# Optimization experiments

Hardware: AMD Instinct MI355X
Metric: run time of the kernel (lower is better)

The kernel has to match this reference:

```python
import jax, jax.numpy as jnp
import numpy as np


def setup_inputs() -> dict:
    key = jax.random.key(0)
    k1, k2, k3, k4 = jax.random.split(key, 4)
    B, C_in, C_out, E, K = 4, 128, 256, 30000, 5
    x = jax.random.normal(k1, (B, C_in, E, 1), dtype=jnp.float32)
    ne_idx = jax.random.randint(k2, (B, E, K - 1), 0, E, dtype=jnp.int32)
    conv_w = jax.random.normal(k3, (C_out, C_in, 1, K), dtype=jnp.float32) * 0.05
    conv_b = jax.random.normal(k4, (C_out,), dtype=jnp.float32) * 0.05
    return {"x": x, "ne_idx": ne_idx, "conv_w": conv_w, "conv_b": conv_b}


def reference(x, ne_idx, conv_w, conv_b):
    # x: [B, C, E, 1] edge features; ne_idx: [B, E, 4] neighbor edge ids.
    B, C, E, _ = x.shape
    xs = x[..., 0]                                        # [B, C, E]

    # pad_graph_mat: prepend self index column -> [B, E, 5]
    self_idx = jnp.broadcast_to(
        jnp.arange(E, dtype=ne_idx.dtype)[None, :, None], (B, E, 1))
    idx = jnp.concatenate([self_idx, ne_idx], axis=2) + 1  # +1 for zero pad slot

    # zero-pad feature dim so index 0 maps to zeros (matches torch padding col)
    x_pad = jnp.pad(xs, ((0, 0), (0, 0), (1, 0)))          # [B, C, E+1]

    # gather: f[b, c, e, k] = x_pad[b, c, idx[b, e, k]]
    f = jax.vmap(lambda xp, i: xp[:, i])(x_pad, idx)       # [B, C, E, 5]

    e0, e1, e2, e3, e4 = (f[..., j] for j in range(5))
    p = e1 + e3
    q = e2 + e4
    p1 = jnp.abs(e1 - e3)
    q1 = jnp.abs(e2 - e4)
    G = jnp.stack([e0, p, q, p1, q1], axis=-1)             # [B, C, E, 5]

    # Conv2d with kernel (1, 5): contraction over in-channels and the 5 taps
    out = jnp.einsum('bcek,ocuk->boe', G, conv_w) + conv_b[None, :, None]
    return out[..., None]                                  # [B, C_out, E, 1]
```

## Files before the change

### kernel.cpp

```cpp
#include <hip/hip_runtime.h>
#include <hip/hip_bf16.h>
#include <stdint.h>

#define E_N   30000
#define C_IN  128
#define C_OUT 256
#define B_N   4
#define KTAP  5
#define BN    64

typedef short bf16x8 __attribute__((ext_vector_type(8)));
typedef float f32x4  __attribute__((ext_vector_type(4)));

static __device__ __forceinline__ unsigned short f2bf(float f) {
    union { float f; uint32_t u; } v; v.f = f;
    uint32_t r = (v.u + 0x7FFFu + ((v.u >> 16) & 1u)) >> 16;
    return (unsigned short)r;
}
static __device__ __forceinline__ float bf2f(uint32_t h) {
    union { uint32_t u; float f; } v; v.u = h << 16;
    return v.f;
}

static __device__ __forceinline__ void comb8(const uint4& u, const uint4& v,
                                             uint4& s, uint4& d) {
    const uint32_t* a = (const uint32_t*)&u;
    const uint32_t* b = (const uint32_t*)&v;
    uint32_t* so = (uint32_t*)&s;
    uint32_t* dr = (uint32_t*)&d;
#pragma unroll
    for (int i = 0; i < 4; ++i) {
        float x0 = bf2f(a[i] & 0xFFFFu), x1 = bf2f(a[i] >> 16);
        float y0 = bf2f(b[i] & 0xFFFFu), y1 = bf2f(b[i] >> 16);
        so[i] = (uint32_t)f2bf(x0 + y0) | ((uint32_t)f2bf(x1 + y1) << 16);
        dr[i] = (uint32_t)f2bf(fabsf(x0 - y0)) | ((uint32_t)f2bf(fabsf(x1 - y1)) << 16);
    }
}

__global__ void pack_w_kernel(const float* __restrict__ w,
                              unsigned short* __restrict__ wp) {
    int tid = blockIdx.x * blockDim.x + threadIdx.x;
    if (tid >= 20 * 16 * 64) return;
    int s    = tid >> 10;
    int mt   = (tid >> 6) & 15;
    int lane = tid & 63;
    int m    = mt * 16 + (lane & 15);
    int kb   = s * 32 + ((lane >> 4) & 3) * 8;
    uint32_t pv[4];
    for (int jj = 0; jj < 4; ++jj) {
        unsigned short lo, hi;
        {
            int kk = kb + 2 * jj;
            int t = kk >> 7, c = kk & 127;
            lo = f2bf(w[(m * C_IN + c) * KTAP + t]);
        }
        {
            int kk = kb + 2 * jj + 1;
            int t = kk >> 7, c = kk & 127;
            hi = f2bf(w[(m * C_IN + c) * KTAP + t]);
        }
        pv[jj] = (uint32_t)lo | ((uint32_t)hi << 16);
    }
    uint4 val; val.x = pv[0]; val.y = pv[1]; val.z = pv[2]; val.w = pv[3];
    *(uint4*)(wp + (size_t)tid * 8) = val;
}

__global__ void transpose_kernel(const float* __restrict__ x,
                                 unsigned short* __restrict__ xT) {
    __shared__ float ld[C_IN][64 + 1];
    int b  = blockIdx.y;
    int e0 = blockIdx.x * 64;
    int t  = threadIdx.x;
    bool full = (e0 + 64 <= E_N);
    for (int pass = 0; pass < 8; ++pass) {
        int c  = pass * 16 + (t >> 4);
        int eo = (t & 15) * 4;
        if (full) {
            const float4 v = *(const float4*)(x + ((size_t)(b * C_IN + c) * E_N + e0 + eo));
            ld[c][eo] = v.x; ld[c][eo + 1] = v.y; ld[c][eo + 2] = v.z; ld[c][eo + 3] = v.w;
        } else {
            for (int i = 0; i < 4; ++i) {
                int e = e0 + eo + i;
                ld[c][eo + i] = (e < E_N) ? x[(size_t)(b * C_IN + c) * E_N + e] : 0.f;
            }
        }
    }
    __syncthreads();
    for (int pass = 0; pass < 4; ++pass) {
        int el = pass * 16 + (t >> 4);
        int c0 = (t & 15) * 8;
        int e  = e0 + el;
        if (e < E_N) {
            uint32_t pk[4];
            for (int i = 0; i < 4; ++i) {
                unsigned short lo = f2bf(ld[c0 + 2 * i][el]);
                unsigned short hi = f2bf(ld[c0 + 2 * i + 1][el]);
                pk[i] = (uint32_t)lo | ((uint32_t)hi << 16);
            }
            uint4 v; v.x = pk[0]; v.y = pk[1]; v.z = pk[2]; v.w = pk[3];
            *(uint4*)(xT + (size_t)(b * E_N + e) * C_IN + c0) = v;
        }
    }
}

__launch_bounds__(512, 4)
__global__ void mesh_gemm(const unsigned short* __restrict__ wp,
                          const unsigned short* __restrict__ xT,
                          const int* __restrict__ ne,
                          const float* __restrict__ bias,
                          float* __restrict__ out) {
    __shared__ uint4 gbuf[KTAP][BN][16];

    const int e0   = blockIdx.x * BN;
    const int tid  = threadIdx.x;
    const int lane = tid & 63;
    const int wave = tid >> 6;
    const int b0   = blockIdx.y * 2;
    const int b1   = b0 + 1;

    const int col = tid >> 3;
    const int ci  = tid & 7;
    int eg = e0 + col; if (eg >= E_N) eg = E_N - 1;

    const int4 nb0 = *(const int4*)(ne + ((size_t)b0 * E_N + eg) * 4);
    const int4 nb1 = *(const int4*)(ne + ((size_t)b1 * E_N + eg) * 4);

    const int sw = col & 15;
    const int cl = ci ^ sw;
    const int ch = (ci + 8) ^ sw;

    const uint4* wp16 = (const uint4*)wp;
    const int nl   = lane & 15;
    const int kq   = lane >> 4;
    const int quad = kq;

    float bvl[2][4];
#pragma unroll
    for (int mt = 0; mt < 2; ++mt)
#pragma unroll
        for (int r = 0; r < 4; ++r)
            bvl[mt][r] = bias[(wave * 2 + mt) * 16 + quad * 4 + r];

    auto gather10 = [&](int b, const int4& nb, uint4* g) {
        const unsigned short* xb = xT + (size_t)b * E_N * C_IN;
        const uint4* r0 = (const uint4*)(xb + (size_t)eg   * C_IN) + ci;
        const uint4* r1 = (const uint4*)(xb + (size_t)nb.x * C_IN) + ci;
        const uint4* r2 = (const uint4*)(xb + (size_t)nb.y * C_IN) + ci;
        const uint4* r3 = (const uint4*)(xb + (size_t)nb.z * C_IN) + ci;
        const uint4* r4 = (const uint4*)(xb + (size_t)nb.w * C_IN) + ci;
        g[0] = r0[0]; g[1] = r1[0]; g[2] = r2[0]; g[3] = r3[0]; g[4] = r4[0];
        g[5] = r0[8]; g[6] = r1[8]; g[7] = r2[8]; g[8] = r3[8]; g[9] = r4[8];
    };
    auto combineStore = [&](uint4* g) {
        uint4 s, d;
        gbuf[0][col][cl] = g[0];
        comb8(g[1], g[3], s, d); gbuf[1][col][cl] = s; gbuf[3][col][cl] = d;
        comb8(g[2], g[4], s, d); gbuf[2][col][cl] = s; gbuf[4][col][cl] = d;
        gbuf[0][col][ch] = g[5];
        comb8(g[6], g[8], s, d); gbuf[1][col][ch] = s; gbuf[3][col][ch] = d;
        comb8(g[7], g[9], s, d); gbuf[2][col][ch] = s; gbuf[4][col][ch] = d;
    };
    auto mfmaStore = [&](int b) {
        f32x4 acc[2][4];
#pragma unroll
        for (int mt = 0; mt < 2; ++mt)
#pragma unroll
            for (int nt = 0; nt < 4; ++nt)
                acc[mt][nt] = (f32x4){0.f, 0.f, 0.f, 0.f};
#pragma unroll 4
        for (int s = 0; s < 20; ++s) {
            const int tap = s >> 2, cbi = s & 3;
            uint4 w0 = wp16[(s * 16 + wave * 2 + 0) * 64 + lane];
            uint4 w1 = wp16[(s * 16 + wave * 2 + 1) * 64 + lane];
            bf16x8 af0 = *(bf16x8*)&w0;
            bf16x8 af1 = *(bf16x8*)&w1;
#pragma unroll
            for (int nt = 0; nt < 4; ++nt) {
                uint4 bv = gbuf[tap][nt * 16 + nl][((cbi << 2) + kq) ^ nl];
                bf16x8 bf = *(bf16x8*)&bv;
                acc[0][nt] = __builtin_amdgcn_mfma_f32_16x16x32_bf16(af0, bf, acc[0][nt], 0, 0, 0);
                acc[1][nt] = __builtin_amdgcn_mfma_f32_16x16x32_bf16(af1, bf, acc[1][nt], 0, 0, 0);
            }
        }
#pragma unroll
        for (int mt = 0; mt < 2; ++mt) {
            const int ob = (wave * 2 + mt) * 16 + quad * 4;
#pragma unroll
            for (int r = 0; r < 4; ++r) {
                const int o = ob + r;
                const float bv = bvl[mt][r];
#pragma unroll
                for (int nt = 0; nt < 4; ++nt) {
                    const int e = e0 + nt * 16 + nl;
                    if (e < E_N)
                        out[((size_t)(b * C_OUT + o)) * E_N + e] = acc[mt][nt][r] + bv;
                }
            }
        }
    };

    uint4 ga[10];
    gather10(b0, nb0, ga);
    combineStore(ga);
    __syncthreads();

    uint4 gb[10];
    gather10(b1, nb1, gb);
    mfmaStore(b0);

    __syncthreads();
    combineStore(gb);
    __syncthreads();
    mfmaStore(b1);
}

__global__ void fallback_kernel(const float* __restrict__ x,
                                const int* __restrict__ ne,
                                const float* __restrict__ w,
                                const float* __restrict__ bias,
                                float* __restrict__ out) {
    size_t id = (size_t)blockIdx.x * blockDim.x + threadIdx.x;
    if (id >= (size_t)B_N * C_OUT * E_N) return;
    int e = (int)(id % E_N);
    int o = (int)((id / E_N) % C_OUT);
    int b = (int)(id / ((size_t)E_N * C_OUT));
    const int4 nb = *(const int4*)(ne + ((size_t)b * E_N + e) * 4);
    float acc = bias[o];
    for (int c = 0; c < C_IN; ++c) {
        const float* xb = x + (size_t)(b * C_IN + c) * E_N;
        float s0 = xb[e];
        float x1 = xb[nb.x], x2 = xb[nb.y], x3 = xb[nb.z], x4 = xb[nb.w];
        const float* wo = w + (size_t)(o * C_IN + c) * KTAP;
        acc += wo[0] * s0
             + wo[1] * (x1 + x3)
             + wo[2] * (x2 + x4)
             + wo[3] * fabsf(x1 - x3)
             + wo[4] * fabsf(x2 - x4);
    }
    out[id] = acc;
}

extern "C" void kernel_launch(void* const* d_in, const int* in_sizes, int n_in,
                              void* d_out, int out_size, void* d_ws, size_t ws_size,
                              hipStream_t stream) {
    const float* x      = (const float*)d_in[0];
    const int*   ne_idx = (const int*)d_in[1];
    const float* conv_w = (const float*)d_in[2];
    const float* conv_b = (const float*)d_in[3];
    float* out = (float*)d_out;

    const size_t xT_off = 512 * 1024;
    const size_t need   = xT_off + (size_t)B_N * E_N * C_IN * 2;

    if (ws_size < need) {
        size_t total = (size_t)B_N * C_OUT * E_N;
        int blocks = (int)((total + 255) / 256);
        fallback_kernel<<<blocks, 256, 0, stream>>>(x, ne_idx, conv_w, conv_b, out);
        return;
    }

    unsigned short* wp = (unsigned short*)d_ws;
    unsigned short* xT = (unsigned short*)((char*)d_ws + xT_off);

    pack_w_kernel<<<80, 256, 0, stream>>>(conv_w, wp);
    dim3 tg((E_N + 63) / 64, B_N);
    transpose_kernel<<<tg, 256, 0, stream>>>(x, xT);
    dim3 gg((E_N + BN - 1) / BN, B_N / 2);
    mesh_gemm<<<gg, 512, 0, stream>>>(wp, xT, ne_idx, conv_b, out);
}
```

Measured before the change: 231.8 us.

## Make mesh_gemm persistent with register-cached weights and software-pipelined gathers

The GEMM kernel now runs as a persistent grid of 512 blocks. Each block loops over (edge-tile, batch) work items in strides of GRIDX and overlaps the gather of the next tile, plus prefetch of its neighbor indices, with the MFMA loop on the current tile. 16 of the 20 weight fragments per wave are loaded once into registers instead of being re-read from global memory every tile, and launch bounds drop to 2 blocks per CU to make room for them. The cost is much higher register pressure and lower occupancy. The fixed 512-block grid also loses the previous per-block reuse of edge indices across two batches.

```diff
diff --git a/kernel.cpp b/kernel.cpp
--- a/kernel.cpp
+++ b/kernel.cpp
@@ -8,6 +8,7 @@
 #define B_N   4
 #define KTAP  5
 #define BN    64
+#define GRIDX 512
 
 typedef short bf16x8 __attribute__((ext_vector_type(8)));
 typedef float f32x4  __attribute__((ext_vector_type(4)));
@@ -103,7 +104,7 @@
     }
 }
 
-__launch_bounds__(512, 4)
+__launch_bounds__(512, 2)
 __global__ void mesh_gemm(const unsigned short* __restrict__ wp,
                           const unsigned short* __restrict__ xT,
                           const int* __restrict__ ne,
@@ -111,38 +112,46 @@
                           float* __restrict__ out) {
     __shared__ uint4 gbuf[KTAP][BN][16];
 
-    const int e0   = blockIdx.x * BN;
     const int tid  = threadIdx.x;
     const int lane = tid & 63;
     const int wave = tid >> 6;
-    const int b0   = blockIdx.y * 2;
-    const int b1   = b0 + 1;
+    const int bq   = blockIdx.x & 3;
+    const int NQ   = ((E_N + BN - 1) / BN) * B_N;
 
     const int col = tid >> 3;
     const int ci  = tid & 7;
-    int eg = e0 + col; if (eg >= E_N) eg = E_N - 1;
-
-    const int4 nb0 = *(const int4*)(ne + ((size_t)b0 * E_N + eg) * 4);
-    const int4 nb1 = *(const int4*)(ne + ((size_t)b1 * E_N + eg) * 4);
-
-    const int sw = col & 15;
-    const int cl = ci ^ sw;
-    const int ch = (ci + 8) ^ sw;
+    const int sw  = col & 15;
+    const int cl  = ci ^ sw;
+    const int ch  = (ci + 8) ^ sw;
+
+    const unsigned short* xb   = xT  + (size_t)bq * E_N * C_IN;
+    const int*            neb  = ne  + (size_t)bq * E_N * 4;
+    float*                outb = out + (size_t)bq * C_OUT * E_N;
 
     const uint4* wp16 = (const uint4*)wp;
-    const int nl   = lane & 15;
-    const int kq   = lane >> 4;
-    const int quad = kq;
+    const int nl = lane & 15;
+    const int kq = lane >> 4;
+
+    uint4 wc0[16], wc1[16];
+#pragma unroll
+    for (int s = 0; s < 16; ++s) {
+        wc0[s] = wp16[(s * 16 + wave * 2 + 0) * 64 + lane];
+        wc1[s] = wp16[(s * 16 + wave * 2 + 1) * 64 + lane];
+    }
 
     float bvl[2][4];
 #pragma unroll
     for (int mt = 0; mt < 2; ++mt)
 #pragma unroll
         for (int r = 0; r < 4; ++r)
-            bvl[mt][r] = bias[(wave * 2 + mt) * 16 + quad * 4 + r];
-
-    auto gather10 = [&](int b, const int4& nb, uint4* g) {
-        const unsigned short* xb = xT + (size_t)b * E_N * C_IN;
+            bvl[mt][r] = bias[(wave * 2 + mt) * 16 + kq * 4 + r];
+
+    auto egOf = [&](int q) {
+        int e = (q >> 2) * BN + col;
+        return (e < E_N) ? e : (E_N - 1);
+    };
+
+    auto gather10 = [&](int eg, const int4& nb, uint4* g) {
         const uint4* r0 = (const uint4*)(xb + (size_t)eg   * C_IN) + ci;
         const uint4* r1 = (const uint4*)(xb + (size_t)nb.x * C_IN) + ci;
         const uint4* r2 = (const uint4*)(xb + (size_t)nb.y * C_IN) + ci;
@@ -160,20 +169,18 @@
         comb8(g[6], g[8], s, d); gbuf[1][col][ch] = s; gbuf[3][col][ch] = d;
         comb8(g[7], g[9], s, d); gbuf[2][col][ch] = s; gbuf[4][col][ch] = d;
     };
-    auto mfmaStore = [&](int b) {
+    auto mfmaStore = [&](int et) {
         f32x4 acc[2][4];
 #pragma unroll
         for (int mt = 0; mt < 2; ++mt)
 #pragma unroll
             for (int nt = 0; nt < 4; ++nt)
                 acc[mt][nt] = (f32x4){0.f, 0.f, 0.f, 0.f};
-#pragma unroll 4
-        for (int s = 0; s < 20; ++s) {
+#pragma unroll
+        for (int s = 0; s < 16; ++s) {
             const int tap = s >> 2, cbi = s & 3;
-            uint4 w0 = wp16[(s * 16 + wave * 2 + 0) * 64 + lane];
-            uint4 w1 = wp16[(s * 16 + wave * 2 + 1) * 64 + lane];
-            bf16x8 af0 = *(bf16x8*)&w0;
-            bf16x8 af1 = *(bf16x8*)&w1;
+            bf16x8 af0 = *(bf16x8*)&wc0[s];
+            bf16x8 af1 = *(bf16x8*)&wc1[s];
 #pragma unroll
             for (int nt = 0; nt < 4; ++nt) {
                 uint4 bv = gbuf[tap][nt * 16 + nl][((cbi << 2) + kq) ^ nl];
@@ -183,8 +190,24 @@
             }
         }
 #pragma unroll
+        for (int s = 16; s < 20; ++s) {
+            const int cbi = s & 3;
+            uint4 w0 = wp16[(s * 16 + wave * 2 + 0) * 64 + lane];
+            uint4 w1 = wp16[(s * 16 + wave * 2 + 1) * 64 + lane];
+            bf16x8 af0 = *(bf16x8*)&w0;
+            bf16x8 af1 = *(bf16x8*)&w1;
+#pragma unroll
+            for (int nt = 0; nt < 4; ++nt) {
+                uint4 bv = gbuf[4][nt * 16 + nl][((cbi << 2) + kq) ^ nl];
+                bf16x8 bf = *(bf16x8*)&bv;
+                acc[0][nt] = __builtin_amdgcn_mfma_f32_16x16x32_bf16(af0, bf, acc[0][nt], 0, 0, 0);
+                acc[1][nt] = __builtin_amdgcn_mfma_f32_16x16x32_bf16(af1, bf, acc[1][nt], 0, 0, 0);
+            }
+        }
+        const int e0 = et * BN;
+#pragma unroll
         for (int mt = 0; mt < 2; ++mt) {
-            const int ob = (wave * 2 + mt) * 16 + quad * 4;
+            const int ob = (wave * 2 + mt) * 16 + kq * 4;
 #pragma unroll
             for (int r = 0; r < 4; ++r) {
                 const int o = ob + r;
@@ -193,25 +216,46 @@
                 for (int nt = 0; nt < 4; ++nt) {
                     const int e = e0 + nt * 16 + nl;
                     if (e < E_N)
-                        out[((size_t)(b * C_OUT + o)) * E_N + e] = acc[mt][nt][r] + bv;
+                        outb[(size_t)o * E_N + e] = acc[mt][nt][r] + bv;
                 }
             }
         }
     };
 
-    uint4 ga[10];
-    gather10(b0, nb0, ga);
-    combineStore(ga);
+    uint4 g[10];
+    int q = blockIdx.x;
+    {
+        int eg = egOf(q);
+        int4 nb = *(const int4*)(neb + (size_t)eg * 4);
+        gather10(eg, nb, g);
+    }
+    int qg = q + GRIDX;
+    int egN = 0; int4 nbN = {0, 0, 0, 0};
+    if (qg < NQ) { egN = egOf(qg); nbN = *(const int4*)(neb + (size_t)egN * 4); }
+
+    combineStore(g);
+    if (qg < NQ) {
+        gather10(egN, nbN, g);
+        int qp = qg + GRIDX;
+        if (qp < NQ) { egN = egOf(qp); nbN = *(const int4*)(neb + (size_t)egN * 4); }
+    }
     __syncthreads();
 
-    uint4 gb[10];
-    gather10(b1, nb1, gb);
-    mfmaStore(b0);
-
-    __syncthreads();
-    combineStore(gb);
-    __syncthreads();
-    mfmaStore(b1);
+    for (;;) {
+        mfmaStore(q >> 2);
+        __syncthreads();
+        const int qc = q + GRIDX;
+        if (qc >= NQ) break;
+        combineStore(g);
+        const int qg2 = qc + GRIDX;
+        if (qg2 < NQ) {
+            gather10(egN, nbN, g);
+            const int qp = qg2 + GRIDX;
+            if (qp < NQ) { egN = egOf(qp); nbN = *(const int4*)(neb + (size_t)egN * 4); }
+        }
+        __syncthreads();
+        q = qc;
+    }
 }
 
 __global__ void fallback_kernel(const float* __restrict__ x,
@@ -265,6 +309,5 @@
     pack_w_kernel<<<80, 256, 0, stream>>>(conv_w, wp);
     dim3 tg((E_N + 63) / 64, B_N);
     transpose_kernel<<<tg, 256, 0, stream>>>(x, xT);
-    dim3 gg((E_N + BN - 1) / BN, B_N / 2);
-    mesh_gemm<<<gg, 512, 0, stream>>>(wp, xT, ne_idx, conv_b, out);
-}
+    mesh_gemm<<<dim3(GRIDX), 512, 0, stream>>>(wp, xT, ne_idx, conv_b, out);
+}
```

Measured after the change: 310.6 us. 1.34x slower.

## Gather both batches into double LDS buffer and share weight loads across batches

Applied to the files above, without the earlier changes.

Both batch items' neighbor gathers are now issued up front into a doubled shared buffer, and a single MFMA loop computes both batches, so each weight fragment loaded from global memory is reused twice. This removes the serialized gather/compute/sync sequence and halves weight reloads. The cost is double the LDS footprint (about 80KB) and twice the accumulator registers, so occupancy is pinned to 2 waves per EU, and latency hiding that came from overlapping the second gather with the first compute is lost.

```diff
diff --git a/kernel.cpp b/kernel.cpp
--- a/kernel.cpp
+++ b/kernel.cpp
@@ -103,46 +103,47 @@
     }
 }
 
-__launch_bounds__(512, 4)
+__launch_bounds__(512)
+__attribute__((amdgpu_waves_per_eu(2, 2)))
 __global__ void mesh_gemm(const unsigned short* __restrict__ wp,
                           const unsigned short* __restrict__ xT,
                           const int* __restrict__ ne,
                           const float* __restrict__ bias,
                           float* __restrict__ out) {
-    __shared__ uint4 gbuf[KTAP][BN][16];
-
-    const int e0   = blockIdx.x * BN;
+    __shared__ uint4 gbuf[2][KTAP][BN][16];
+
     const int tid  = threadIdx.x;
     const int lane = tid & 63;
     const int wave = tid >> 6;
+    const int e0   = blockIdx.x * BN;
     const int b0   = blockIdx.y * 2;
     const int b1   = b0 + 1;
 
     const int col = tid >> 3;
     const int ci  = tid & 7;
+    const int sw  = col & 15;
+    const int cl  = ci ^ sw;
+    const int ch  = (ci + 8) ^ sw;
     int eg = e0 + col; if (eg >= E_N) eg = E_N - 1;
 
     const int4 nb0 = *(const int4*)(ne + ((size_t)b0 * E_N + eg) * 4);
     const int4 nb1 = *(const int4*)(ne + ((size_t)b1 * E_N + eg) * 4);
 
-    const int sw = col & 15;
-    const int cl = ci ^ sw;
-    const int ch = (ci + 8) ^ sw;
+    const unsigned short* xb0 = xT + (size_t)b0 * E_N * C_IN;
+    const unsigned short* xb1 = xT + (size_t)b1 * E_N * C_IN;
 
     const uint4* wp16 = (const uint4*)wp;
-    const int nl   = lane & 15;
-    const int kq   = lane >> 4;
-    const int quad = kq;
+    const int nl = lane & 15;
+    const int kq = lane >> 4;
 
     float bvl[2][4];
 #pragma unroll
     for (int mt = 0; mt < 2; ++mt)
 #pragma unroll
         for (int r = 0; r < 4; ++r)
-            bvl[mt][r] = bias[(wave * 2 + mt) * 16 + quad * 4 + r];
-
-    auto gather10 = [&](int b, const int4& nb, uint4* g) {
-        const unsigned short* xb = xT + (size_t)b * E_N * C_IN;
+            bvl[mt][r] = bias[(wave * 2 + mt) * 16 + kq * 4 + r];
+
+    auto gather10 = [&](const unsigned short* xb, const int4& nb, uint4* g) {
         const uint4* r0 = (const uint4*)(xb + (size_t)eg   * C_IN) + ci;
         const uint4* r1 = (const uint4*)(xb + (size_t)nb.x * C_IN) + ci;
         const uint4* r2 = (const uint4*)(xb + (size_t)nb.y * C_IN) + ci;
@@ -151,40 +152,61 @@
         g[0] = r0[0]; g[1] = r1[0]; g[2] = r2[0]; g[3] = r3[0]; g[4] = r4[0];
         g[5] = r0[8]; g[6] = r1[8]; g[7] = r2[8]; g[8] = r3[8]; g[9] = r4[8];
     };
-    auto combineStore = [&](uint4* g) {
+    auto combineStore = [&](const uint4* g, int bh) {
         uint4 s, d;
-        gbuf[0][col][cl] = g[0];
-        comb8(g[1], g[3], s, d); gbuf[1][col][cl] = s; gbuf[3][col][cl] = d;
-        comb8(g[2], g[4], s, d); gbuf[2][col][cl] = s; gbuf[4][col][cl] = d;
-        gbuf[0][col][ch] = g[5];
-        comb8(g[6], g[8], s, d); gbuf[1][col][ch] = s; gbuf[3][col][ch] = d;
-        comb8(g[7], g[9], s, d); gbuf[2][col][ch] = s; gbuf[4][col][ch] = d;
+        gbuf[bh][0][col][cl] = g[0];
+        comb8(g[1], g[3], s, d); gbuf[bh][1][col][cl] = s; gbuf[bh][3][col][cl] = d;
+        comb8(g[2], g[4], s, d); gbuf[bh][2][col][cl] = s; gbuf[bh][4][col][cl] = d;
+        gbuf[bh][0][col][ch] = g[5];
+        comb8(g[6], g[8], s, d); gbuf[bh][1][col][ch] = s; gbuf[bh][3][col][ch] = d;
+        comb8(g[7], g[9], s, d); gbuf[bh][2][col][ch] = s; gbuf[bh][4][col][ch] = d;
     };
-    auto mfmaStore = [&](int b) {
-        f32x4 acc[2][4];
+
+    {
+        uint4 g0[10], g1[10];
+        gather10(xb0, nb0, g0);
+        gather10(xb1, nb1, g1);
+        combineStore(g0, 0);
+        combineStore(g1, 1);
+    }
+    __syncthreads();
+
+    f32x4 acc[2][2][4];
+#pragma unroll
+    for (int bh = 0; bh < 2; ++bh)
 #pragma unroll
         for (int mt = 0; mt < 2; ++mt)
 #pragma unroll
             for (int nt = 0; nt < 4; ++nt)
-                acc[mt][nt] = (f32x4){0.f, 0.f, 0.f, 0.f};
+                acc[bh][mt][nt] = (f32x4){0.f, 0.f, 0.f, 0.f};
+
 #pragma unroll 4
-        for (int s = 0; s < 20; ++s) {
-            const int tap = s >> 2, cbi = s & 3;
-            uint4 w0 = wp16[(s * 16 + wave * 2 + 0) * 64 + lane];
-            uint4 w1 = wp16[(s * 16 + wave * 2 + 1) * 64 + lane];
-            bf16x8 af0 = *(bf16x8*)&w0;
-            bf16x8 af1 = *(bf16x8*)&w1;
-#pragma unroll
-            for (int nt = 0; nt < 4; ++nt) {
-                uint4 bv = gbuf[tap][nt * 16 + nl][((cbi << 2) + kq) ^ nl];
-                bf16x8 bf = *(bf16x8*)&bv;
-                acc[0][nt] = __builtin_amdgcn_mfma_f32_16x16x32_bf16(af0, bf, acc[0][nt], 0, 0, 0);
-                acc[1][nt] = __builtin_amdgcn_mfma_f32_16x16x32_bf16(af1, bf, acc[1][nt], 0, 0, 0);
-            }
-        }
+    for (int s = 0; s < 20; ++s) {
+        const int tap = s >> 2, cbi = s & 3;
+        uint4 w0 = wp16[(s * 16 + wave * 2 + 0) * 64 + lane];
+        uint4 w1 = wp16[(s * 16 + wave * 2 + 1) * 64 + lane];
+        bf16x8 af0 = *(bf16x8*)&w0;
+        bf16x8 af1 = *(bf16x8*)&w1;
+#pragma unroll
+        for (int nt = 0; nt < 4; ++nt) {
+            const int cidx = ((cbi << 2) + kq) ^ nl;
+            uint4 bv0 = gbuf[0][tap][nt * 16 + nl][cidx];
+            bf16x8 bf0 = *(bf16x8*)&bv0;
+            acc[0][0][nt] = __builtin_amdgcn_mfma_f32_16x16x32_bf16(af0, bf0, acc[0][0][nt], 0, 0, 0);
+            acc[0][1][nt] = __builtin_amdgcn_mfma_f32_16x16x32_bf16(af1, bf0, acc[0][1][nt], 0, 0, 0);
+            uint4 bv1 = gbuf[1][tap][nt * 16 + nl][cidx];
+            bf16x8 bf1 = *(bf16x8*)&bv1;
+            acc[1][0][nt] = __builtin_amdgcn_mfma_f32_16x16x32_bf16(af0, bf1, acc[1][0][nt], 0, 0, 0);
+            acc[1][1][nt] = __builtin_amdgcn_mfma_f32_16x16x32_bf16(af1, bf1, acc[1][1][nt], 0, 0, 0);
+        }
+    }
+
+#pragma unroll
+    for (int bh = 0; bh < 2; ++bh) {
+        float* outb = out + (size_t)(b0 + bh) * C_OUT * E_N;
 #pragma unroll
         for (int mt = 0; mt < 2; ++mt) {
-            const int ob = (wave * 2 + mt) * 16 + quad * 4;
+            const int ob = (wave * 2 + mt) * 16 + kq * 4;
 #pragma unroll
             for (int r = 0; r < 4; ++r) {
                 const int o = ob + r;
@@ -193,25 +215,11 @@
                 for (int nt = 0; nt < 4; ++nt) {
                     const int e = e0 + nt * 16 + nl;
                     if (e < E_N)
-                        out[((size_t)(b * C_OUT + o)) * E_N + e] = acc[mt][nt][r] + bv;
+                        outb[(size_t)o * E_N + e] = acc[bh][mt][nt][r] + bv;
                 }
             }
         }
-    };
-
-    uint4 ga[10];
-    gather10(b0, nb0, ga);
-    combineStore(ga);
-    __syncthreads();
-
-    uint4 gb[10];
-    gather10(b1, nb1, gb);
-    mfmaStore(b0);
-
-    __syncthreads();
-    combineStore(gb);
-    __syncthreads();
-    mfmaStore(b1);
+    }
 }
 
 __global__ void fallback_kernel(const float* __restrict__ x,
```

New measurement: 244.7 us. +5.6%, slower.

## Split gather into channel halves to halve LDS and registers, raise occupancy

Applied to the files above, without the earlier changes.

The shared gather buffer now holds only half of the input channels, and the single batch's work is processed as two K-halves accumulated into the same registers. Only five gathered vectors are live at a time instead of ten. This cuts LDS and VGPR use so more waves per EU fit (waves_per_eu 6), while the next half's global gather still overlaps the MFMA loop. MFMA sections get raised scheduling priority. The cost is twice as many block barriers and more frequent LDS round trips, and bias is now read at store time.

```diff
diff --git a/kernel.cpp b/kernel.cpp
--- a/kernel.cpp
+++ b/kernel.cpp
@@ -103,115 +103,130 @@
     }
 }
 
-__launch_bounds__(512, 4)
+__launch_bounds__(512)
+__attribute__((amdgpu_waves_per_eu(6)))
 __global__ void mesh_gemm(const unsigned short* __restrict__ wp,
                           const unsigned short* __restrict__ xT,
                           const int* __restrict__ ne,
                           const float* __restrict__ bias,
                           float* __restrict__ out) {
-    __shared__ uint4 gbuf[KTAP][BN][16];
-
-    const int e0   = blockIdx.x * BN;
+    __shared__ uint4 gbuf[KTAP][BN][8];
+
     const int tid  = threadIdx.x;
     const int lane = tid & 63;
     const int wave = tid >> 6;
+    const int e0   = blockIdx.x * BN;
     const int b0   = blockIdx.y * 2;
-    const int b1   = b0 + 1;
 
     const int col = tid >> 3;
     const int ci  = tid & 7;
+    const int cs  = ci ^ (col & 7);
     int eg = e0 + col; if (eg >= E_N) eg = E_N - 1;
 
-    const int4 nb0 = *(const int4*)(ne + ((size_t)b0 * E_N + eg) * 4);
-    const int4 nb1 = *(const int4*)(ne + ((size_t)b1 * E_N + eg) * 4);
-
-    const int sw = col & 15;
-    const int cl = ci ^ sw;
-    const int ch = (ci + 8) ^ sw;
+    const unsigned short* xb0 = xT + (size_t)b0 * E_N * C_IN;
+    const unsigned short* xb1 = xb0 + (size_t)E_N * C_IN;
 
     const uint4* wp16 = (const uint4*)wp;
-    const int nl   = lane & 15;
-    const int kq   = lane >> 4;
-    const int quad = kq;
-
-    float bvl[2][4];
-#pragma unroll
-    for (int mt = 0; mt < 2; ++mt)
-#pragma unroll
-        for (int r = 0; r < 4; ++r)
-            bvl[mt][r] = bias[(wave * 2 + mt) * 16 + quad * 4 + r];
-
-    auto gather10 = [&](int b, const int4& nb, uint4* g) {
-        const unsigned short* xb = xT + (size_t)b * E_N * C_IN;
-        const uint4* r0 = (const uint4*)(xb + (size_t)eg   * C_IN) + ci;
-        const uint4* r1 = (const uint4*)(xb + (size_t)nb.x * C_IN) + ci;
-        const uint4* r2 = (const uint4*)(xb + (size_t)nb.y * C_IN) + ci;
-        const uint4* r3 = (const uint4*)(xb + (size_t)nb.z * C_IN) + ci;
-        const uint4* r4 = (const uint4*)(xb + (size_t)nb.w * C_IN) + ci;
-        g[0] = r0[0]; g[1] = r1[0]; g[2] = r2[0]; g[3] = r3[0]; g[4] = r4[0];
-        g[5] = r0[8]; g[6] = r1[8]; g[7] = r2[8]; g[8] = r3[8]; g[9] = r4[8];
-    };
-    auto combineStore = [&](uint4* g) {
+    const int nl = lane & 15;
+    const int kq = lane >> 4;
+
+    auto gather5 = [&](const unsigned short* xb, const int4& nb, int h, uint4* g) {
+        const int off = ci + (h << 3);
+        g[0] = ((const uint4*)(xb + (size_t)eg   * C_IN))[off];
+        g[1] = ((const uint4*)(xb + (size_t)nb.x * C_IN))[off];
+        g[2] = ((const uint4*)(xb + (size_t)nb.y * C_IN))[off];
+        g[3] = ((const uint4*)(xb + (size_t)nb.z * C_IN))[off];
+        g[4] = ((const uint4*)(xb + (size_t)nb.w * C_IN))[off];
+    };
+    auto combineStore5 = [&](const uint4* g) {
         uint4 s, d;
-        gbuf[0][col][cl] = g[0];
-        comb8(g[1], g[3], s, d); gbuf[1][col][cl] = s; gbuf[3][col][cl] = d;
-        comb8(g[2], g[4], s, d); gbuf[2][col][cl] = s; gbuf[4][col][cl] = d;
-        gbuf[0][col][ch] = g[5];
-        comb8(g[6], g[8], s, d); gbuf[1][col][ch] = s; gbuf[3][col][ch] = d;
-        comb8(g[7], g[9], s, d); gbuf[2][col][ch] = s; gbuf[4][col][ch] = d;
-    };
-    auto mfmaStore = [&](int b) {
-        f32x4 acc[2][4];
-#pragma unroll
-        for (int mt = 0; mt < 2; ++mt)
-#pragma unroll
-            for (int nt = 0; nt < 4; ++nt)
-                acc[mt][nt] = (f32x4){0.f, 0.f, 0.f, 0.f};
+        gbuf[0][col][cs] = g[0];
+        comb8(g[1], g[3], s, d); gbuf[1][col][cs] = s; gbuf[3][col][cs] = d;
+        comb8(g[2], g[4], s, d); gbuf[2][col][cs] = s; gbuf[4][col][cs] = d;
+    };
+    auto mfmaHalf = [&](int h, f32x4 (&acc)[2][4]) {
+        __builtin_amdgcn_s_setprio(1);
 #pragma unroll 4
-        for (int s = 0; s < 20; ++s) {
-            const int tap = s >> 2, cbi = s & 3;
+        for (int p = 0; p < 10; ++p) {
+            const int tap = p >> 1, cbi2 = p & 1;
+            const int s = tap * 4 + (h << 1) + cbi2;
             uint4 w0 = wp16[(s * 16 + wave * 2 + 0) * 64 + lane];
             uint4 w1 = wp16[(s * 16 + wave * 2 + 1) * 64 + lane];
             bf16x8 af0 = *(bf16x8*)&w0;
             bf16x8 af1 = *(bf16x8*)&w1;
 #pragma unroll
             for (int nt = 0; nt < 4; ++nt) {
-                uint4 bv = gbuf[tap][nt * 16 + nl][((cbi << 2) + kq) ^ nl];
+                uint4 bv = gbuf[tap][nt * 16 + nl][((cbi2 << 2) + kq) ^ (nl & 7)];
                 bf16x8 bf = *(bf16x8*)&bv;
                 acc[0][nt] = __builtin_amdgcn_mfma_f32_16x16x32_bf16(af0, bf, acc[0][nt], 0, 0, 0);
                 acc[1][nt] = __builtin_amdgcn_mfma_f32_16x16x32_bf16(af1, bf, acc[1][nt], 0, 0, 0);
             }
         }
+        __builtin_amdgcn_s_setprio(0);
+    };
+    auto storeOut = [&](int b, f32x4 (&acc)[2][4]) {
+        float* outb = out + (size_t)b * C_OUT * E_N;
 #pragma unroll
         for (int mt = 0; mt < 2; ++mt) {
-            const int ob = (wave * 2 + mt) * 16 + quad * 4;
+            const int ob = (wave * 2 + mt) * 16 + kq * 4;
 #pragma unroll
             for (int r = 0; r < 4; ++r) {
                 const int o = ob + r;
-                const float bv = bvl[mt][r];
+                const float bv = bias[o];
 #pragma unroll
                 for (int nt = 0; nt < 4; ++nt) {
                     const int e = e0 + nt * 16 + nl;
                     if (e < E_N)
-                        out[((size_t)(b * C_OUT + o)) * E_N + e] = acc[mt][nt][r] + bv;
+                        outb[(size_t)o * E_N + e] = acc[mt][nt][r] + bv;
                 }
             }
         }
     };
 
-    uint4 ga[10];
-    gather10(b0, nb0, ga);
-    combineStore(ga);
-    __syncthreads();
-
-    uint4 gb[10];
-    gather10(b1, nb1, gb);
-    mfmaStore(b0);
-
-    __syncthreads();
-    combineStore(gb);
-    __syncthreads();
-    mfmaStore(b1);
+    f32x4 acc[2][4];
+    uint4 g[5];
+
+    const int4 nb0 = *(const int4*)(ne + ((size_t)b0 * E_N + eg) * 4);
+
+    gather5(xb0, nb0, 0, g);
+    combineStore5(g);
+    __syncthreads();
+
+    const int4 nb1 = *(const int4*)(ne + ((size_t)(b0 + 1) * E_N + eg) * 4);
+    gather5(xb0, nb0, 1, g);
+#pragma unroll
+    for (int mt = 0; mt < 2; ++mt)
+#pragma unroll
+        for (int nt = 0; nt < 4; ++nt)
+            acc[mt][nt] = (f32x4){0.f, 0.f, 0.f, 0.f};
+    mfmaHalf(0, acc);
+    __syncthreads();
+
+    combineStore5(g);
+    __syncthreads();
+
+    gather5(xb1, nb1, 0, g);
+    mfmaHalf(1, acc);
+    storeOut(b0, acc);
+    __syncthreads();
+
+    combineStore5(g);
+    __syncthreads();
+
+    gather5(xb1, nb1, 1, g);
+#pragma unroll
+    for (int mt = 0; mt < 2; ++mt)
+#pragma unroll
+        for (int nt = 0; nt < 4; ++nt)
+            acc[mt][nt] = (f32x4){0.f, 0.f, 0.f, 0.f};
+    mfmaHalf(0, acc);
+    __syncthreads();
+
+    combineStore5(g);
+    __syncthreads();
+
+    mfmaHalf(1, acc);
+    storeOut(b0 + 1, acc);
 }
 
 __global__ void fallback_kernel(const float* __restrict__ x,
```

Result: slower. 334.9 us (+44.5%).
